# Optimization experiments

Hardware: AMD Instinct MI355X
Metric: run time of the kernel (lower is better)

Reference implementation:

```python
import jax, jax.numpy as jnp
import numpy as np

WS, OWS, HEADS, DH = 8, 12, 4, 16
INNER = HEADS * DH
DIM = 64
RATIO = 0.5
REL = 12  # rel_size = WS + (OWS - WS)


def _conv1x1(x, W, b):
    return jnp.einsum('oc,bchw->bohw', W, x) + b[None, :, None, None]


def _lrelu(x):
    return jnp.where(x >= 0, x, 0.1 * x)


def _rel_to_abs(x):
    # x: [b, l, 2r-1] -> [b, l, r]
    b, l, m = x.shape
    r = (m + 1) // 2
    x = jnp.pad(x, ((0, 0), (0, 0), (0, 1))).reshape(b, l * (m + 1))
    x = jnp.pad(x, ((0, 0), (0, m - l))).reshape(b, l + 1, m)
    return x[:, :l, -r:]


def _relative_logits_1d(q, rel_k):
    # q: [b, h, w, d], rel_k: [2r-1, d] -> [b, h, r, w, r]
    b, h, w, _ = q.shape
    r = (rel_k.shape[0] + 1) // 2
    logits = jnp.einsum('bxyd,rd->bxyr', q, rel_k)
    logits = _rel_to_abs(logits.reshape(b * h, w, 2 * r - 1)).reshape(b, h, w, r)
    return jnp.broadcast_to(logits[:, :, None], (b, h, r, w, r))


def _rel_pos_emb(q, rel_h, rel_w):
    # q: [b, WS*WS, DH] -> [b, WS*WS, REL*REL]
    b = q.shape[0]
    q = q.reshape(b, WS, WS, DH)
    lw = _relative_logits_1d(q, rel_w)                        # [b, x, i, y, j]
    lw = lw.transpose(0, 1, 3, 2, 4).reshape(b, WS * WS, REL * REL)   # (x y),(i j)
    lh = _relative_logits_1d(q.transpose(0, 2, 1, 3), rel_h)  # [b, y, i, x, j]
    lh = lh.transpose(0, 3, 1, 4, 2).reshape(b, WS * WS, REL * REL)   # (x y),(j i)
    return lw + lh


def _windows(t, B, Hw, Ww):
    # 'b c (h p1) (w p2) -> b (h w) (p1 p2 c)'
    return t.reshape(B, INNER, Hw, WS, Ww, WS).transpose(0, 2, 4, 3, 5, 1).reshape(B, Hw * Ww, WS * WS * INNER)


def _forward(x, condition_global, Wq, bq, Wk, bk, Wv, bv, Wout, bout,
             rel_h, rel_w, pin_W, pin_b, ln_w, ln_b, sa_W, sa_b,
             m1_W, m1_b, m2_W, m2_b):
    B, C, H, W = x.shape
    Hw, Ww = H // WS, W // WS
    Nw = Hw * Ww
    keep = int(Nw * RATIO)  # deterministic num_keep_node (expected r=0.5)
    scale = DH ** -0.5

    qs = _conv1x1(x, Wq, bq)
    ks = _conv1x1(x, Wk, bk)
    vs = _conv1x1(x, Wv, bv)

    # condition_wind: stacked ij meshgrid of linspace(-1,1,WS), tiled over windows
    lin = jnp.linspace(-1.0, 1.0, WS)
    gy, gx = jnp.meshgrid(lin, lin, indexing='ij')
    wind = jnp.tile(jnp.stack([gy, gx]).astype(x.dtype)[None], (B, 1, Hw, Ww))
    cond = jnp.concatenate([vs, condition_global, wind], axis=1)  # [B, INNER+4, H, W]

    # PredictorLG
    h1 = _conv1x1(cond, pin_W, pin_b)
    u = h1.mean(1, keepdims=True)
    s = ((h1 - u) ** 2).mean(1, keepdims=True)
    h1 = ln_w[None, :, None, None] * (h1 - u) / jnp.sqrt(s + 1e-6) + ln_b[None, :, None, None]
    h1 = _lrelu(h1)
    sa = jax.lax.conv_general_dilated(h1, sa_W, (1, 1), ((1, 1), (1, 1)),
                                      dimension_numbers=('NCHW', 'OIHW', 'NCHW'))
    sa = jax.nn.sigmoid(sa + sa_b[None, :, None, None])          # [B,1,H,W]

    xm = h1.mean(1)                                               # [B,H,W]
    xm = xm.reshape(B, Hw, WS, Ww, WS).transpose(0, 1, 3, 2, 4).reshape(B, Nw, WS * WS)
    z = _lrelu(xm @ m1_W.T + m1_b)
    pred = jax.nn.softmax(z @ m2_W.T + m2_b, axis=-1)
    score = pred[:, :, 0]
    idx = jnp.argsort(-score, axis=1)
    idx1, idx2 = idx[:, :keep], idx[:, keep:]
    bar = jnp.arange(B)[:, None]

    v_easy = vs * sa

    qw = _windows(qs, B, Hw, Ww)                                  # [B, Nw, 64*INNER]

    pad = (OWS - WS) // 2
    def unfold(t):
        p = jax.lax.conv_general_dilated_patches(t, (OWS, OWS), (WS, WS),
                                                 [(pad, pad), (pad, pad)])
        # [B, INNER*OWS*OWS, Hw, Ww], channel-major (c, kh, kw) like torch unfold
        p = p.reshape(B, INNER, OWS * OWS, Nw)
        return p.transpose(0, 3, 2, 1).reshape(B, Nw, OWS * OWS * INNER)  # (j c)
    kw, vw = unfold(ks), unfold(vs)

    qk, kk, vk = qw[bar, idx1], kw[bar, idx1], vw[bar, idx1]       # gather hard windows

    def heads(t, ntok):
        return t.reshape(B * keep, ntok, HEADS, DH).transpose(0, 2, 1, 3).reshape(B * keep * HEADS, ntok, DH)
    qh = heads(qk, WS * WS) * scale
    kh = heads(kk, OWS * OWS)
    vh = heads(vk, OWS * OWS)

    attn = jnp.einsum('bqc,bkc->bqk', qh, kh) + _rel_pos_emb(qh, rel_h, rel_w)
    attn = jax.nn.softmax(attn, axis=-1)
    vo = jnp.einsum('bqk,bkc->bqc', attn, vh)                      # [B*keep*HEADS, 64, DH]

    # '(b j head) (p1 p2) c -> b j (p1 p2 head c)'
    v1 = vo.reshape(B, keep, HEADS, WS * WS, DH).transpose(0, 1, 3, 2, 4).reshape(B, keep, WS * WS * INNER)
    v2 = _windows(v_easy, B, Hw, Ww)[bar, idx2]

    out = jnp.zeros((B, Nw, WS * WS * INNER), x.dtype)
    out = out.at[bar, idx1].set(v1).at[bar, idx2].set(v2)          # batch_index_fill
    # 'b (h w) (dh dw c) -> b c (h dh) (w dw)'
    out = out.reshape(B, Hw, Ww, WS, WS, INNER).transpose(0, 5, 1, 3, 2, 4).reshape(B, INNER, H, W)
    return _conv1x1(out, Wout, bout)


def setup_inputs() -> dict:
    key = jax.random.key(0)
    k = jax.random.split(key, 16)
    B, H, W = 2, 256, 256
    cdim = INNER + 4
    rel_scale = DH ** -0.5

    def p(kk, shape, s=0.05):
        return jax.random.normal(kk, shape, jnp.float32) * s

    return {
        'x': jax.random.normal(k[0], (B, DIM, H, W), jnp.float32),
        'condition_global': jax.random.normal(k[1], (B, 2, H, W), jnp.float32),
        'Wq': p(k[2], (INNER, DIM)), 'bq': jnp.zeros((INNER,), jnp.float32),
        'Wk': p(k[3], (INNER, DIM)), 'bk': jnp.zeros((INNER,), jnp.float32),
        'Wv': p(k[4], (INNER, DIM)), 'bv': jnp.zeros((INNER,), jnp.float32),
        'Wout': p(k[5], (DIM, INNER)), 'bout': jnp.zeros((DIM,), jnp.float32),
        'rel_h': jax.random.normal(k[6], (2 * REL - 1, DH), jnp.float32) * rel_scale,
        'rel_w': jax.random.normal(k[7], (2 * REL - 1, DH), jnp.float32) * rel_scale,
        'pin_W': p(k[8], (cdim // 4, cdim)), 'pin_b': jnp.zeros((cdim // 4,), jnp.float32),
        'ln_w': jnp.ones((cdim // 4,), jnp.float32), 'ln_b': jnp.zeros((cdim // 4,), jnp.float32),
        'sa_W': p(k[9], (1, cdim // 4, 3, 3)), 'sa_b': jnp.zeros((1,), jnp.float32),
        'm1_W': p(k[10], (WS, WS * WS)), 'm1_b': jnp.zeros((WS,), jnp.float32),
        'm2_W': p(k[11], (2, WS)), 'm2_b': jnp.zeros((2,), jnp.float32),
    }


def reference(x, condition_global, Wq, bq, Wk, bk, Wv, bv, Wout, bout,
              rel_h, rel_w, pin_W, pin_b, ln_w, ln_b, sa_W, sa_b,
              m1_W, m1_b, m2_W, m2_b):
    return _forward(x, condition_global, Wq, bq, Wk, bk, Wv, bv, Wout, bout,
                    rel_h, rel_w, pin_W, pin_b, ln_w, ln_b, sa_W, sa_b,
                    m1_W, m1_b, m2_W, m2_b)
```

## Files before the change

### kernel.cpp

```cpp
#include <hip/hip_runtime.h>
#include <math.h>

#define NPIX   65536
#define NPIXT  131072
#define NW     1024
#define KEEP   512
#define PITCH  68


__global__ __launch_bounds__(256) void k_qkv(
    const float* __restrict__ x,
    const float* __restrict__ Wq, const float* __restrict__ bq,
    const float* __restrict__ Wk, const float* __restrict__ bk,
    const float* __restrict__ Wv, const float* __restrict__ bv,
    float* __restrict__ qs, float* __restrict__ ks, float* __restrict__ vs)
{
    __shared__ float xs[64][64];
    const int tid  = threadIdx.x;
    const int px   = tid & 63;
    const int og   = __builtin_amdgcn_readfirstlane(tid >> 6);
    const int tile = blockIdx.x;
    const int b    = tile >> 10;
    const int p0   = (tile & 1023) << 6;
    const int gp   = (b << 16) + p0 + px;

    #pragma unroll
    for (int it = 0; it < 4; ++it) {
        const int i = it * 256 + tid;
        const int c = i >> 4;
        const int f = i & 15;
        *(float4*)&xs[c][f * 4] =
            *(const float4*)(x + ((size_t)(b * 64 + c)) * NPIX + p0 + f * 4);
    }
    __syncthreads();

    const float* Ws[3]   = {Wq, Wk, Wv};
    const float* bias[3] = {bq, bk, bv};
    float* outs[3] = {qs + (size_t)gp * 64, ks + (size_t)gp * 64, vs + (size_t)gp * 64};

    float acc[3][16];
    #pragma unroll
    for (int m = 0; m < 3; ++m)
        #pragma unroll
        for (int j = 0; j < 16; ++j) acc[m][j] = 0.f;

    #pragma unroll 2
    for (int c = 0; c < 64; ++c) {
        const float xv = xs[c][px];
        #pragma unroll
        for (int m = 0; m < 3; ++m) {
            const float* W = Ws[m];
            #pragma unroll
            for (int j = 0; j < 16; ++j)
                acc[m][j] += W[(og * 16 + j) * 64 + c] * xv;
        }
    }
    #pragma unroll
    for (int m = 0; m < 3; ++m) {
        const float* bb = bias[m];
        #pragma unroll
        for (int j4 = 0; j4 < 4; ++j4) {
            float4 v;
            v.x = acc[m][j4 * 4 + 0] + bb[og * 16 + j4 * 4 + 0];
            v.y = acc[m][j4 * 4 + 1] + bb[og * 16 + j4 * 4 + 1];
            v.z = acc[m][j4 * 4 + 2] + bb[og * 16 + j4 * 4 + 2];
            v.w = acc[m][j4 * 4 + 3] + bb[og * 16 + j4 * 4 + 3];
            *(float4*)(outs[m] + og * 16 + j4 * 4) = v;
        }
    }
}

__global__ __launch_bounds__(256) void k_cond(
    const float* __restrict__ vs, const float* __restrict__ cg,
    const float* __restrict__ pinW, const float* __restrict__ pinb,
    const float* __restrict__ lnw, const float* __restrict__ lnb,
    float* __restrict__ h1, float* __restrict__ xm)
{
    const int gp = blockIdx.x * 256 + threadIdx.x;
    const int b  = gp >> 16;
    const int p  = gp & 65535;
    const int h  = p >> 8;
    const int w  = p & 255;

    float acc[17];
    #pragma unroll
    for (int oc = 0; oc < 17; ++oc) acc[oc] = pinb[oc];

    const float* vp = vs + (size_t)gp * 64;
    #pragma unroll 4
    for (int c4 = 0; c4 < 16; ++c4) {
        const float4 v4 = *(const float4*)(vp + c4 * 4);
        const float vv[4] = {v4.x, v4.y, v4.z, v4.w};
        #pragma unroll
        for (int k = 0; k < 4; ++k) {
            const int c = c4 * 4 + k;
            #pragma unroll
            for (int oc = 0; oc < 17; ++oc)
                acc[oc] += pinW[oc * 68 + c] * vv[k];
        }
    }
    const float c64 = cg[(b * 2 + 0) * NPIX + p];
    const float c65 = cg[(b * 2 + 1) * NPIX + p];
    const float c66 = -1.f + 2.f * (float)(h & 7) / 7.f;
    const float c67 = -1.f + 2.f * (float)(w & 7) / 7.f;
    #pragma unroll
    for (int oc = 0; oc < 17; ++oc)
        acc[oc] += pinW[oc * 68 + 64] * c64 + pinW[oc * 68 + 65] * c65 +
                   pinW[oc * 68 + 66] * c66 + pinW[oc * 68 + 67] * c67;

    float u = 0.f;
    #pragma unroll
    for (int oc = 0; oc < 17; ++oc) u += acc[oc];
    u *= (1.f / 17.f);
    float s = 0.f;
    #pragma unroll
    for (int oc = 0; oc < 17; ++oc) { const float d = acc[oc] - u; s += d * d; }
    s *= (1.f / 17.f);
    const float rstd = rsqrtf(s + 1e-6f);

    float xsum = 0.f;
    #pragma unroll
    for (int oc = 0; oc < 17; ++oc) {
        float hv = lnw[oc] * (acc[oc] - u) * rstd + lnb[oc];
        hv = (hv >= 0.f) ? hv : 0.1f * hv;
        h1[(b * 17 + oc) * NPIX + p] = hv;
        xsum += hv;
    }
    xm[gp] = xsum * (1.f / 17.f);
}

__global__ __launch_bounds__(256) void k_sa(
    const float* __restrict__ h1, const float* __restrict__ saW,
    const float* __restrict__ sab, float* __restrict__ sa)
{
    __shared__ float S[17 * 3 * 256];
    const int tid = threadIdx.x;
    const int b   = blockIdx.x >> 8;
    const int row = blockIdx.x & 255;

    for (int i = tid; i < 3264; i += 256) {
        const int ch  = i / 192;
        const int rem = i - ch * 192;
        const int dr  = rem >> 6;
        const int c4  = rem & 63;
        const int rr  = row + dr - 1;
        float4 v = {0.f, 0.f, 0.f, 0.f};
        if ((unsigned)rr < 256u)
            v = *(const float4*)(h1 + ((size_t)(b * 17 + ch)) * NPIX + rr * 256 + c4 * 4);
        *(float4*)&S[(ch * 3 + dr) * 256 + c4 * 4] = v;
    }
    __syncthreads();

    const int w = tid;
    float acc = sab[0];
    #pragma unroll 1
    for (int ch = 0; ch < 17; ++ch) {
        #pragma unroll
        for (int dr = 0; dr < 3; ++dr) {
            const float* Sp = &S[(ch * 3 + dr) * 256];
            const float m  = Sp[w];
            const float l  = (w > 0)   ? Sp[w - 1] : 0.f;
            const float r_ = (w < 255) ? Sp[w + 1] : 0.f;
            const float* Wp = saW + (ch * 3 + dr) * 3;
            acc += Wp[0] * l + Wp[1] * m + Wp[2] * r_;
        }
    }
    sa[b * NPIX + row * 256 + w] = 1.f / (1.f + __expf(-acc));
}

__global__ __launch_bounds__(1024) void k_score_select(
    const float* __restrict__ xm,
    const float* __restrict__ m1W, const float* __restrict__ m1b,
    const float* __restrict__ m2W, const float* __restrict__ m2b,
    int* __restrict__ flag, int* __restrict__ kept)
{
    __shared__ float sc[NW];
    const int b = blockIdx.x;
    const int t = threadIdx.x;
    const int i = t >> 5;
    const int j = t & 31;

    float z[8];
    #pragma unroll
    for (int jj = 0; jj < 8; ++jj) z[jj] = m1b[jj];

    for (int a = 0; a < 8; ++a) {
        #pragma unroll
        for (int cc = 0; cc < 8; ++cc) {
            const float xv = xm[b * NPIX + (i * 8 + a) * 256 + (j * 8 + cc)];
            const int tt = a * 8 + cc;
            #pragma unroll
            for (int jj = 0; jj < 8; ++jj)
                z[jj] += m1W[jj * 64 + tt] * xv;
        }
    }
    #pragma unroll
    for (int jj = 0; jj < 8; ++jj) z[jj] = (z[jj] >= 0.f) ? z[jj] : 0.1f * z[jj];

    float l0 = m2b[0], l1 = m2b[1];
    #pragma unroll
    for (int jj = 0; jj < 8; ++jj) { l0 += m2W[jj] * z[jj]; l1 += m2W[8 + jj] * z[jj]; }
    const float mx = fmaxf(l0, l1);
    const float e0 = expf(l0 - mx), e1 = expf(l1 - mx);
    sc[t] = e0 / (e0 + e1);
    __syncthreads();

    const float s = sc[t];
    int cnt = 0;
    for (int jq = 0; jq < NW; ++jq) {
        const float sj = sc[jq];
        cnt += (sj > s) || (sj == s && jq < t);
    }
    flag[b * NW + t] = (cnt < KEEP) ? 1 : 0;
    if (cnt < KEEP) kept[b * KEEP + cnt] = t;
}

__global__ __launch_bounds__(256) void k_attn(
    const float* __restrict__ qs, const float* __restrict__ ks,
    const float* __restrict__ vs, const int* __restrict__ kept,
    const float* __restrict__ relh, const float* __restrict__ relw,
    float* __restrict__ amix)
{
    __shared__ float SK[72 * PITCH];
    __shared__ float SV[72 * PITCH];

    const int b    = blockIdx.y;
    const int win  = kept[b * KEEP + blockIdx.x];
    const int wy = win >> 5, wx = win & 31;
    const int tid  = threadIdx.x;
    const int head = tid >> 6;
    const int lane = tid & 63;
    const int choff = head * 16;
    const size_t bbase = (size_t)b * NPIX;
    const int px0 = (wy * 8) * 256 + wx * 8;

    #pragma unroll
    for (int it = 0; it < 4; ++it) {
        const int i  = it * 256 + tid;
        const int px = i >> 4;
        const int c4 = i & 15;
        const float4 v = *(const float4*)(
            qs + (bbase + px0 + (px >> 3) * 256 + (px & 7)) * 64 + c4 * 4);
        *(float4*)&SK[px * PITCH + c4 * 4] = v;
    }
    __syncthreads();

    const int qrow = lane >> 3, qcol = lane & 7;
    float q[16];
    #pragma unroll
    for (int j4 = 0; j4 < 4; ++j4) {
        const float4 v = *(const float4*)&SK[(qrow * 8 + qcol) * PITCH + choff + j4 * 4];
        q[j4 * 4 + 0] = v.x * 0.25f; q[j4 * 4 + 1] = v.y * 0.25f;
        q[j4 * 4 + 2] = v.z * 0.25f; q[j4 * 4 + 3] = v.w * 0.25f;
    }

    float cw[12];
    #pragma unroll
    for (int k = 0; k < 12; ++k) {
        const float* rw = relw + (k - qcol + 11) * 16;
        float sw = 0.f;
        #pragma unroll
        for (int j4 = 0; j4 < 4; ++j4) {
            const float4 w4 = *(const float4*)(rw + j4 * 4);
            sw += q[j4*4+0]*w4.x + q[j4*4+1]*w4.y + q[j4*4+2]*w4.z + q[j4*4+3]*w4.w;
        }
        cw[k] = sw;
    }

    const int wy8 = wy * 8 - 2, wx8 = wx * 8 - 2;

    float sum = 0.f;
    float vo[16];
    #pragma unroll
    for (int d = 0; d < 16; ++d) vo[d] = 0.f;

    #pragma unroll 1
    for (int c = 0; c < 2; ++c) {
        __syncthreads();
        for (int i = tid; i < 1152; i += 256) {
            const int pxl = i >> 4;
            const int c4  = i & 15;
            const int rl  = pxl / 12;
            const int col = pxl - rl * 12;
            const int ry  = wy8 + 6 * c + rl;
            const int cx  = wx8 + col;
            float4 kv = {0.f,0.f,0.f,0.f}, vv = {0.f,0.f,0.f,0.f};
            if ((unsigned)ry < 256u && (unsigned)cx < 256u) {
                const size_t g = (bbase + ry * 256 + cx) * 64 + c4 * 4;
                kv = *(const float4*)(ks + g);
                vv = *(const float4*)(vs + g);
            }
            *(float4*)&SK[pxl * PITCH + c4 * 4] = kv;
            *(float4*)&SV[pxl * PITCH + c4 * 4] = vv;
        }
        __syncthreads();

        #pragma unroll 1
        for (int rl = 0; rl < 6; ++rl) {
            const float* rh = relh + (c * 6 + rl - qrow + 11) * 16;
            float srow = 0.f;
            #pragma unroll
            for (int j4 = 0; j4 < 4; ++j4) {
                const float4 h4 = *(const float4*)(rh + j4 * 4);
                srow += q[j4*4+0]*h4.x + q[j4*4+1]*h4.y + q[j4*4+2]*h4.z + q[j4*4+3]*h4.w;
            }

            const float* kbase = &SK[(rl * 12) * PITCH + choff];
            const float* vbase = &SV[(rl * 12) * PITCH + choff];
            #pragma unroll
            for (int col = 0; col < 12; ++col) {
                const float* kb = kbase + col * PITCH;
                const float4 k0 = *(const float4*)(kb + 0);
                const float4 k1 = *(const float4*)(kb + 4);
                const float4 k2 = *(const float4*)(kb + 8);
                const float4 k3 = *(const float4*)(kb + 12);
                float s = srow + cw[col];
                s += k0.x*q[0];  s += k0.y*q[1];  s += k0.z*q[2];  s += k0.w*q[3];
                s += k1.x*q[4];  s += k1.y*q[5];  s += k1.z*q[6];  s += k1.w*q[7];
                s += k2.x*q[8];  s += k2.y*q[9];  s += k2.z*q[10]; s += k2.w*q[11];
                s += k3.x*q[12]; s += k3.y*q[13]; s += k3.z*q[14]; s += k3.w*q[15];
                const float e = __expf(s);
                sum += e;
                const float* vb = vbase + col * PITCH;
                const float4 v0 = *(const float4*)(vb + 0);
                const float4 v1 = *(const float4*)(vb + 4);
                const float4 v2 = *(const float4*)(vb + 8);
                const float4 v3 = *(const float4*)(vb + 12);
                vo[0]  += e*v0.x; vo[1]  += e*v0.y; vo[2]  += e*v0.z; vo[3]  += e*v0.w;
                vo[4]  += e*v1.x; vo[5]  += e*v1.y; vo[6]  += e*v1.z; vo[7]  += e*v1.w;
                vo[8]  += e*v2.x; vo[9]  += e*v2.y; vo[10] += e*v2.z; vo[11] += e*v2.w;
                vo[12] += e*v3.x; vo[13] += e*v3.y; vo[14] += e*v3.z; vo[15] += e*v3.w;
            }
        }
    }

    const float inv = 1.f / sum;
    __syncthreads();
    #pragma unroll
    for (int j4 = 0; j4 < 4; ++j4) {
        float4 v;
        v.x = vo[j4*4+0] * inv; v.y = vo[j4*4+1] * inv;
        v.z = vo[j4*4+2] * inv; v.w = vo[j4*4+3] * inv;
        *(float4*)&SK[(qrow * 8 + qcol) * PITCH + choff + j4 * 4] = v;
    }
    __syncthreads();
    #pragma unroll
    for (int it = 0; it < 4; ++it) {
        const int i  = it * 256 + tid;
        const int px = i >> 4;
        const int c4 = i & 15;
        const float4 v = *(const float4*)&SK[px * PITCH + c4 * 4];
        *(float4*)(amix + (bbase + px0 + (px >> 3) * 256 + (px & 7)) * 64 + c4 * 4) = v;
    }
}

__global__ __launch_bounds__(256) void k_out_f(
    const float* __restrict__ amix, const float* __restrict__ vs,
    const float* __restrict__ sa, const int* __restrict__ flag,
    const float* __restrict__ W, const float* __restrict__ bias,
    float* __restrict__ out)
{
    __shared__ float xs[64][65];
    __shared__ float smult[64];
    __shared__ int   sflag[64];
    const int tid  = threadIdx.x;
    const int px   = tid & 63;
    const int og   = __builtin_amdgcn_readfirstlane(tid >> 6);
    const int tile = blockIdx.x;
    const int b    = tile >> 10;
    const int p0   = (tile & 1023) << 6;
    const int p    = p0 + px;
    const int gp   = (b << 16) + p;

    {
        const int h   = p >> 8, w = p & 255;
        const int win = (h >> 3) * 32 + (w >> 3);
        const int fl  = flag[b * NW + win];
        sflag[px] = fl;
        smult[px] = fl ? 1.f : sa[gp];
    }
    __syncthreads();

    #pragma unroll
    for (int it = 0; it < 4; ++it) {
        const int i   = it * 256 + tid;
        const int pxl = i >> 4;
        const int c4  = i & 15;
        const int gpl = (b << 16) + p0 + pxl;
        const float* src = (sflag[pxl] ? amix : vs) + (size_t)gpl * 64;
        const float m = smult[pxl];
        const float4 v = *(const float4*)(src + c4 * 4);
        xs[c4 * 4 + 0][pxl] = v.x * m;
        xs[c4 * 4 + 1][pxl] = v.y * m;
        xs[c4 * 4 + 2][pxl] = v.z * m;
        xs[c4 * 4 + 3][pxl] = v.w * m;
    }
    __syncthreads();

    float acc[16];
    #pragma unroll
    for (int j = 0; j < 16; ++j) acc[j] = 0.f;
    #pragma unroll 2
    for (int c = 0; c < 64; ++c) {
        const float xv = xs[c][px];
        #pragma unroll
        for (int j = 0; j < 16; ++j)
            acc[j] += W[(og * 16 + j) * 64 + c] * xv;
    }

    const int base = (b << 6) * NPIX + p;
    #pragma unroll
    for (int j = 0; j < 16; ++j)
        out[base + (og * 16 + j) * NPIX] = acc[j] + bias[og * 16 + j];
}

extern "C" void kernel_launch(void* const* d_in, const int* in_sizes, int n_in,
                              void* d_out, int out_size, void* d_ws, size_t ws_size,
                              hipStream_t stream)
{
    const float* x    = (const float*)d_in[0];
    const float* cg   = (const float*)d_in[1];
    const float* Wq   = (const float*)d_in[2];
    const float* bq   = (const float*)d_in[3];
    const float* Wk   = (const float*)d_in[4];
    const float* bk   = (const float*)d_in[5];
    const float* Wv   = (const float*)d_in[6];
    const float* bv   = (const float*)d_in[7];
    const float* Wout = (const float*)d_in[8];
    const float* bout = (const float*)d_in[9];
    const float* relh = (const float*)d_in[10];
    const float* relw = (const float*)d_in[11];
    const float* pinW = (const float*)d_in[12];
    const float* pinb = (const float*)d_in[13];
    const float* lnw  = (const float*)d_in[14];
    const float* lnb  = (const float*)d_in[15];
    const float* saW  = (const float*)d_in[16];
    const float* sab  = (const float*)d_in[17];
    const float* m1W  = (const float*)d_in[18];
    const float* m1b  = (const float*)d_in[19];
    const float* m2W  = (const float*)d_in[20];
    const float* m2b  = (const float*)d_in[21];
    float* out = (float*)d_out;

    float* ws    = (float*)d_ws;
    float* qs    = ws;
    float* ks    = qs + 8388608;
    float* vs    = ks + 8388608;
    float* h1    = vs + 8388608;
    float* xm    = h1 + 17 * NPIXT;
    float* sa    = xm + NPIXT;
    int*   flag  = (int*)(sa + NPIXT);
    int*   kept  = flag + 2048;

    k_qkv         <<<2048, 256, 0, stream>>>(x, Wq, bq, Wk, bk, Wv, bv, qs, ks, vs);
    k_cond        <<<NPIXT / 256, 256, 0, stream>>>(vs, cg, pinW, pinb, lnw, lnb, h1, xm);
    k_sa          <<<512, 256, 0, stream>>>(h1, saW, sab, sa);
    k_score_select<<<2, 1024, 0, stream>>>(xm, m1W, m1b, m2W, m2b, flag, kept);
    k_attn        <<<dim3(KEEP, 2), 256, 0, stream>>>(qs, ks, vs, kept, relh, relw, qs);
    k_out_f       <<<2048, 256, 0, stream>>>(qs, vs, sa, flag, Wout, bout, out);
}
```

Measured before the change: 377.4 us.

## Stage transposed weights in LDS, shrink attention LDS, vectorize top-k ranking

The QKV and output projections now transpose the weight matrix into shared memory and read it as float4 rows. Before, each thread issued scalar global (or scalar-cache) weight loads. The QKV kernel also streams x straight from global with register prefetch instead of staging a tile. The attention kernel loads q directly from global and splits the K/V halo into four smaller chunks, halving shared memory so more blocks can be resident. The top-k ranking loop reads scores as float4, and one unroll factor is raised. Costs are extra barriers per chunk, and the QKV path now reads x from global three times and reloads weights per matrix.

```diff
diff --git a/kernel.cpp b/kernel.cpp
--- a/kernel.cpp
+++ b/kernel.cpp
@@ -15,7 +15,7 @@
     const float* __restrict__ Wv, const float* __restrict__ bv,
     float* __restrict__ qs, float* __restrict__ ks, float* __restrict__ vs)
 {
-    __shared__ float xs[64][64];
+    __shared__ float Wt[64][68];
     const int tid  = threadIdx.x;
     const int px   = tid & 63;
     const int og   = __builtin_amdgcn_readfirstlane(tid >> 6);
@@ -24,48 +24,74 @@
     const int p0   = (tile & 1023) << 6;
     const int gp   = (b << 16) + p0 + px;
 
-    #pragma unroll
-    for (int it = 0; it < 4; ++it) {
-        const int i = it * 256 + tid;
-        const int c = i >> 4;
-        const int f = i & 15;
-        *(float4*)&xs[c][f * 4] =
-            *(const float4*)(x + ((size_t)(b * 64 + c)) * NPIX + p0 + f * 4);
-    }
-    __syncthreads();
-
     const float* Ws[3]   = {Wq, Wk, Wv};
     const float* bias[3] = {bq, bk, bv};
     float* outs[3] = {qs + (size_t)gp * 64, ks + (size_t)gp * 64, vs + (size_t)gp * 64};
-
-    float acc[3][16];
-    #pragma unroll
-    for (int m = 0; m < 3; ++m)
-        #pragma unroll
-        for (int j = 0; j < 16; ++j) acc[m][j] = 0.f;
-
-    #pragma unroll 2
-    for (int c = 0; c < 64; ++c) {
-        const float xv = xs[c][px];
-        #pragma unroll
-        for (int m = 0; m < 3; ++m) {
-            const float* W = Ws[m];
+    const float* xg = x + ((size_t)b * 64) * NPIX + p0 + px;
+    const int wo = og * 16;
+
+    #pragma unroll
+    for (int m = 0; m < 3; ++m) {
+        __syncthreads();
+        const float* Wm = Ws[m];
+        #pragma unroll
+        for (int it = 0; it < 4; ++it) {
+            const int i  = it * 256 + tid;
+            const int o  = i >> 4;
+            const int c4 = i & 15;
+            const float4 w = *(const float4*)(Wm + o * 64 + c4 * 4);
+            Wt[c4 * 4 + 0][o] = w.x;
+            Wt[c4 * 4 + 1][o] = w.y;
+            Wt[c4 * 4 + 2][o] = w.z;
+            Wt[c4 * 4 + 3][o] = w.w;
+        }
+        __syncthreads();
+
+        float acc[16];
+        #pragma unroll
+        for (int j = 0; j < 16; ++j) acc[j] = 0.f;
+
+        float xr[8];
+        #pragma unroll
+        for (int k = 0; k < 8; ++k) xr[k] = xg[(size_t)k * NPIX];
+
+        #pragma unroll 2
+        for (int cb = 0; cb < 64; cb += 8) {
+            float xn[8];
+            if (cb + 8 < 64) {
+                #pragma unroll
+                for (int k = 0; k < 8; ++k) xn[k] = xg[(size_t)(cb + 8 + k) * NPIX];
+            }
             #pragma unroll
-            for (int j = 0; j < 16; ++j)
-                acc[m][j] += W[(og * 16 + j) * 64 + c] * xv;
-        }
-    }
-    #pragma unroll
-    for (int m = 0; m < 3; ++m) {
+            for (int k = 0; k < 8; ++k) {
+                const int c = cb + k;
+                const float xv = xr[k];
+                const float4 w0 = *(const float4*)&Wt[c][wo + 0];
+                const float4 w1 = *(const float4*)&Wt[c][wo + 4];
+                const float4 w2 = *(const float4*)&Wt[c][wo + 8];
+                const float4 w3 = *(const float4*)&Wt[c][wo + 12];
+                acc[0]  += w0.x * xv; acc[1]  += w0.y * xv;
+                acc[2]  += w0.z * xv; acc[3]  += w0.w * xv;
+                acc[4]  += w1.x * xv; acc[5]  += w1.y * xv;
+                acc[6]  += w1.z * xv; acc[7]  += w1.w * xv;
+                acc[8]  += w2.x * xv; acc[9]  += w2.y * xv;
+                acc[10] += w2.z * xv; acc[11] += w2.w * xv;
+                acc[12] += w3.x * xv; acc[13] += w3.y * xv;
+                acc[14] += w3.z * xv; acc[15] += w3.w * xv;
+            }
+            #pragma unroll
+            for (int k = 0; k < 8; ++k) xr[k] = xn[k];
+        }
+
         const float* bb = bias[m];
         #pragma unroll
         for (int j4 = 0; j4 < 4; ++j4) {
             float4 v;
-            v.x = acc[m][j4 * 4 + 0] + bb[og * 16 + j4 * 4 + 0];
-            v.y = acc[m][j4 * 4 + 1] + bb[og * 16 + j4 * 4 + 1];
-            v.z = acc[m][j4 * 4 + 2] + bb[og * 16 + j4 * 4 + 2];
-            v.w = acc[m][j4 * 4 + 3] + bb[og * 16 + j4 * 4 + 3];
-            *(float4*)(outs[m] + og * 16 + j4 * 4) = v;
+            v.x = acc[j4 * 4 + 0] + bb[wo + j4 * 4 + 0];
+            v.y = acc[j4 * 4 + 1] + bb[wo + j4 * 4 + 1];
+            v.z = acc[j4 * 4 + 2] + bb[wo + j4 * 4 + 2];
+            v.w = acc[j4 * 4 + 3] + bb[wo + j4 * 4 + 3];
+            *(float4*)(outs[m] + wo + j4 * 4) = v;
         }
     }
 }
@@ -87,7 +113,7 @@
     for (int oc = 0; oc < 17; ++oc) acc[oc] = pinb[oc];
 
     const float* vp = vs + (size_t)gp * 64;
-    #pragma unroll 4
+    #pragma unroll 8
     for (int c4 = 0; c4 < 16; ++c4) {
         const float4 v4 = *(const float4*)(vp + c4 * 4);
         const float vv[4] = {v4.x, v4.y, v4.z, v4.w};
@@ -207,9 +233,12 @@
 
     const float s = sc[t];
     int cnt = 0;
-    for (int jq = 0; jq < NW; ++jq) {
-        const float sj = sc[jq];
-        cnt += (sj > s) || (sj == s && jq < t);
+    for (int jq = 0; jq < NW; jq += 4) {
+        const float4 s4 = *(const float4*)&sc[jq];
+        cnt += (s4.x > s) || (s4.x == s && (jq + 0) < t);
+        cnt += (s4.y > s) || (s4.y == s && (jq + 1) < t);
+        cnt += (s4.z > s) || (s4.z == s && (jq + 2) < t);
+        cnt += (s4.w > s) || (s4.w == s && (jq + 3) < t);
     }
     flag[b * NW + t] = (cnt < KEEP) ? 1 : 0;
     if (cnt < KEEP) kept[b * KEEP + cnt] = t;
@@ -221,8 +250,9 @@
     const float* __restrict__ relh, const float* __restrict__ relw,
     float* __restrict__ amix)
 {
-    __shared__ float SK[72 * PITCH];
-    __shared__ float SV[72 * PITCH];
+    __shared__ float S[2 * 36 * PITCH];
+    float* SK = S;
+    float* SV = S + 36 * PITCH;
 
     const int b    = blockIdx.y;
     const int win  = kept[b * KEEP + blockIdx.x];
@@ -233,25 +263,17 @@
     const int choff = head * 16;
     const size_t bbase = (size_t)b * NPIX;
     const int px0 = (wy * 8) * 256 + wx * 8;
-
-    #pragma unroll
-    for (int it = 0; it < 4; ++it) {
-        const int i  = it * 256 + tid;
-        const int px = i >> 4;
-        const int c4 = i & 15;
-        const float4 v = *(const float4*)(
-            qs + (bbase + px0 + (px >> 3) * 256 + (px & 7)) * 64 + c4 * 4);
-        *(float4*)&SK[px * PITCH + c4 * 4] = v;
-    }
-    __syncthreads();
-
     const int qrow = lane >> 3, qcol = lane & 7;
+
     float q[16];
-    #pragma unroll
-    for (int j4 = 0; j4 < 4; ++j4) {
-        const float4 v = *(const float4*)&SK[(qrow * 8 + qcol) * PITCH + choff + j4 * 4];
-        q[j4 * 4 + 0] = v.x * 0.25f; q[j4 * 4 + 1] = v.y * 0.25f;
-        q[j4 * 4 + 2] = v.z * 0.25f; q[j4 * 4 + 3] = v.w * 0.25f;
+    {
+        const float* qp = qs + (bbase + px0 + qrow * 256 + qcol) * 64 + choff;
+        #pragma unroll
+        for (int j4 = 0; j4 < 4; ++j4) {
+            const float4 v = *(const float4*)(qp + j4 * 4);
+            q[j4 * 4 + 0] = v.x * 0.25f; q[j4 * 4 + 1] = v.y * 0.25f;
+            q[j4 * 4 + 2] = v.z * 0.25f; q[j4 * 4 + 3] = v.w * 0.25f;
+        }
     }
 
     float cw[12];
@@ -275,14 +297,14 @@
     for (int d = 0; d < 16; ++d) vo[d] = 0.f;
 
     #pragma unroll 1
-    for (int c = 0; c < 2; ++c) {
+    for (int cc = 0; cc < 4; ++cc) {
         __syncthreads();
-        for (int i = tid; i < 1152; i += 256) {
+        for (int i = tid; i < 576; i += 256) {
             const int pxl = i >> 4;
             const int c4  = i & 15;
             const int rl  = pxl / 12;
             const int col = pxl - rl * 12;
-            const int ry  = wy8 + 6 * c + rl;
+            const int ry  = wy8 + 3 * cc + rl;
             const int cx  = wx8 + col;
             float4 kv = {0.f,0.f,0.f,0.f}, vv = {0.f,0.f,0.f,0.f};
             if ((unsigned)ry < 256u && (unsigned)cx < 256u) {
@@ -296,8 +318,8 @@
         __syncthreads();
 
         #pragma unroll 1
-        for (int rl = 0; rl < 6; ++rl) {
-            const float* rh = relh + (c * 6 + rl - qrow + 11) * 16;
+        for (int rl = 0; rl < 3; ++rl) {
+            const float* rh = relh + (3 * cc + rl - qrow + 11) * 16;
             float srow = 0.f;
             #pragma unroll
             for (int j4 = 0; j4 < 4; ++j4) {
@@ -341,7 +363,7 @@
         float4 v;
         v.x = vo[j4*4+0] * inv; v.y = vo[j4*4+1] * inv;
         v.z = vo[j4*4+2] * inv; v.w = vo[j4*4+3] * inv;
-        *(float4*)&SK[(qrow * 8 + qcol) * PITCH + choff + j4 * 4] = v;
+        *(float4*)&S[(qrow * 8 + qcol) * PITCH + choff + j4 * 4] = v;
     }
     __syncthreads();
     #pragma unroll
@@ -349,7 +371,7 @@
         const int i  = it * 256 + tid;
         const int px = i >> 4;
         const int c4 = i & 15;
-        const float4 v = *(const float4*)&SK[px * PITCH + c4 * 4];
+        const float4 v = *(const float4*)&S[px * PITCH + c4 * 4];
         *(float4*)(amix + (bbase + px0 + (px >> 3) * 256 + (px & 7)) * 64 + c4 * 4) = v;
     }
 }
@@ -361,6 +383,7 @@
     float* __restrict__ out)
 {
     __shared__ float xs[64][65];
+    __shared__ float Wt[64][68];
     __shared__ float smult[64];
     __shared__ int   sflag[64];
     const int tid  = threadIdx.x;
@@ -371,10 +394,23 @@
     const int p0   = (tile & 1023) << 6;
     const int p    = p0 + px;
     const int gp   = (b << 16) + p;
+    const int wo   = og * 16;
+
+    #pragma unroll
+    for (int it = 0; it < 4; ++it) {
+        const int i  = it * 256 + tid;
+        const int o  = i >> 4;
+        const int c4 = i & 15;
+        const float4 w = *(const float4*)(W + o * 64 + c4 * 4);
+        Wt[c4 * 4 + 0][o] = w.x;
+        Wt[c4 * 4 + 1][o] = w.y;
+        Wt[c4 * 4 + 2][o] = w.z;
+        Wt[c4 * 4 + 3][o] = w.w;
+    }
 
     {
-        const int h   = p >> 8, w = p & 255;
-        const int win = (h >> 3) * 32 + (w >> 3);
+        const int h   = p >> 8, w_ = p & 255;
+        const int win = (h >> 3) * 32 + (w_ >> 3);
         const int fl  = flag[b * NW + win];
         sflag[px] = fl;
         smult[px] = fl ? 1.f : sa[gp];
@@ -400,18 +436,27 @@
     float acc[16];
     #pragma unroll
     for (int j = 0; j < 16; ++j) acc[j] = 0.f;
-    #pragma unroll 2
+    #pragma unroll 4
     for (int c = 0; c < 64; ++c) {
         const float xv = xs[c][px];
-        #pragma unroll
-        for (int j = 0; j < 16; ++j)
-            acc[j] += W[(og * 16 + j) * 64 + c] * xv;
+        const float4 w0 = *(const float4*)&Wt[c][wo + 0];
+        const float4 w1 = *(const float4*)&Wt[c][wo + 4];
+        const float4 w2 = *(const float4*)&Wt[c][wo + 8];
+        const float4 w3 = *(const float4*)&Wt[c][wo + 12];
+        acc[0]  += w0.x * xv; acc[1]  += w0.y * xv;
+        acc[2]  += w0.z * xv; acc[3]  += w0.w * xv;
+        acc[4]  += w1.x * xv; acc[5]  += w1.y * xv;
+        acc[6]  += w1.z * xv; acc[7]  += w1.w * xv;
+        acc[8]  += w2.x * xv; acc[9]  += w2.y * xv;
+        acc[10] += w2.z * xv; acc[11] += w2.w * xv;
+        acc[12] += w3.x * xv; acc[13] += w3.y * xv;
+        acc[14] += w3.z * xv; acc[15] += w3.w * xv;
     }
 
     const int base = (b << 6) * NPIX + p;
     #pragma unroll
     for (int j = 0; j < 16; ++j)
-        out[base + (og * 16 + j) * NPIX] = acc[j] + bias[og * 16 + j];
+        out[base + (wo + j) * NPIX] = acc[j] + bias[wo + j];
 }
 
 extern "C" void kernel_launch(void* const* d_in, const int* in_sizes, int n_in,
```

Result: faster. 366.4 us (-2.9%).

## Rework QKV, attention and output kernels with lane-broadcast weights and two pixels per thread

Applied to the files above, without the earlier changes.

The QKV and output projections now hold weights in registers and broadcast them across the wavefront with readlane. Each thread computes two pixels, and QKV reads x directly from global memory instead of staging it in LDS. Attention moves to one 64-thread block per head, drops its LDS staging, and loads K/V per lane and broadcasts them via readlane. xm is written in window-major order so score selection can use float4 loads, and the rank loop is vectorised. These changes aim to cut LDS traffic and syncs, at the risk of many scalar readlane operations and less coalesced K/V loads.

```diff
diff --git a/kernel.cpp b/kernel.cpp
--- a/kernel.cpp
+++ b/kernel.cpp
@@ -5,8 +5,11 @@
 #define NPIXT  131072
 #define NW     1024
 #define KEEP   512
-#define PITCH  68
-
+
+
+__device__ __forceinline__ float bcast(float v, int l) {
+    return __int_as_float(__builtin_amdgcn_readlane(__float_as_int(v), l));
+}
 
 __global__ __launch_bounds__(256) void k_qkv(
     const float* __restrict__ x,
@@ -15,57 +18,54 @@
     const float* __restrict__ Wv, const float* __restrict__ bv,
     float* __restrict__ qs, float* __restrict__ ks, float* __restrict__ vs)
 {
-    __shared__ float xs[64][64];
     const int tid  = threadIdx.x;
-    const int px   = tid & 63;
+    const int lane = tid & 63;
     const int og   = __builtin_amdgcn_readfirstlane(tid >> 6);
     const int tile = blockIdx.x;
-    const int b    = tile >> 10;
-    const int p0   = (tile & 1023) << 6;
-    const int gp   = (b << 16) + p0 + px;
-
-    #pragma unroll
-    for (int it = 0; it < 4; ++it) {
-        const int i = it * 256 + tid;
-        const int c = i >> 4;
-        const int f = i & 15;
-        *(float4*)&xs[c][f * 4] =
-            *(const float4*)(x + ((size_t)(b * 64 + c)) * NPIX + p0 + f * 4);
-    }
-    __syncthreads();
+    const int b    = tile >> 9;
+    const int p0   = (tile & 511) << 7;
+    const int p    = p0 + 2 * lane;
+    const int gp   = (b << 16) + p;
+    const int wo   = og * 16;
 
     const float* Ws[3]   = {Wq, Wk, Wv};
     const float* bias[3] = {bq, bk, bv};
     float* outs[3] = {qs + (size_t)gp * 64, ks + (size_t)gp * 64, vs + (size_t)gp * 64};
-
-    float acc[3][16];
-    #pragma unroll
-    for (int m = 0; m < 3; ++m)
-        #pragma unroll
-        for (int j = 0; j < 16; ++j) acc[m][j] = 0.f;
-
-    #pragma unroll 2
-    for (int c = 0; c < 64; ++c) {
-        const float xv = xs[c][px];
-        #pragma unroll
-        for (int m = 0; m < 3; ++m) {
-            const float* W = Ws[m];
+    const float* xg = x + ((size_t)b * 64) * NPIX + p;
+
+    #pragma unroll
+    for (int m = 0; m < 3; ++m) {
+        const float* Wm = Ws[m];
+        float w[16];
+        #pragma unroll
+        for (int j = 0; j < 16; ++j) w[j] = Wm[(wo + j) * 64 + lane];
+
+        float acc0[16], acc1[16];
+        #pragma unroll
+        for (int j = 0; j < 16; ++j) { acc0[j] = 0.f; acc1[j] = 0.f; }
+
+        #pragma unroll 8
+        for (int c = 0; c < 64; ++c) {
+            const float2 xv = *(const float2*)(xg + (size_t)c * NPIX);
             #pragma unroll
-            for (int j = 0; j < 16; ++j)
-                acc[m][j] += W[(og * 16 + j) * 64 + c] * xv;
-        }
-    }
-    #pragma unroll
-    for (int m = 0; m < 3; ++m) {
+            for (int j = 0; j < 16; ++j) {
+                const float wv = bcast(w[j], c);
+                acc0[j] += wv * xv.x;
+                acc1[j] += wv * xv.y;
+            }
+        }
+
         const float* bb = bias[m];
+        float* o0 = outs[m];
         #pragma unroll
         for (int j4 = 0; j4 < 4; ++j4) {
-            float4 v;
-            v.x = acc[m][j4 * 4 + 0] + bb[og * 16 + j4 * 4 + 0];
-            v.y = acc[m][j4 * 4 + 1] + bb[og * 16 + j4 * 4 + 1];
-            v.z = acc[m][j4 * 4 + 2] + bb[og * 16 + j4 * 4 + 2];
-            v.w = acc[m][j4 * 4 + 3] + bb[og * 16 + j4 * 4 + 3];
-            *(float4*)(outs[m] + og * 16 + j4 * 4) = v;
+            float4 v0, v1;
+            v0.x = acc0[j4*4+0] + bb[wo + j4*4+0]; v1.x = acc1[j4*4+0] + bb[wo + j4*4+0];
+            v0.y = acc0[j4*4+1] + bb[wo + j4*4+1]; v1.y = acc1[j4*4+1] + bb[wo + j4*4+1];
+            v0.z = acc0[j4*4+2] + bb[wo + j4*4+2]; v1.z = acc1[j4*4+2] + bb[wo + j4*4+2];
+            v0.w = acc0[j4*4+3] + bb[wo + j4*4+3]; v1.w = acc1[j4*4+3] + bb[wo + j4*4+3];
+            *(float4*)(o0 + wo + j4*4)      = v0;
+            *(float4*)(o0 + 64 + wo + j4*4) = v1;
         }
     }
 }
@@ -87,7 +87,7 @@
     for (int oc = 0; oc < 17; ++oc) acc[oc] = pinb[oc];
 
     const float* vp = vs + (size_t)gp * 64;
-    #pragma unroll 4
+    #pragma unroll 8
     for (int c4 = 0; c4 < 16; ++c4) {
         const float4 v4 = *(const float4*)(vp + c4 * 4);
         const float vv[4] = {v4.x, v4.y, v4.z, v4.w};
@@ -126,7 +126,9 @@
         h1[(b * 17 + oc) * NPIX + p] = hv;
         xsum += hv;
     }
-    xm[gp] = xsum * (1.f / 17.f);
+    const int win = (h >> 3) * 32 + (w >> 3);
+    const int idx = ((h & 7) << 3) | (w & 7);
+    xm[(b << 16) + win * 64 + idx] = xsum * (1.f / 17.f);
 }
 
 __global__ __launch_bounds__(256) void k_sa(
@@ -177,21 +179,22 @@
     __shared__ float sc[NW];
     const int b = blockIdx.x;
     const int t = threadIdx.x;
-    const int i = t >> 5;
-    const int j = t & 31;
 
     float z[8];
     #pragma unroll
     for (int jj = 0; jj < 8; ++jj) z[jj] = m1b[jj];
 
-    for (int a = 0; a < 8; ++a) {
-        #pragma unroll
-        for (int cc = 0; cc < 8; ++cc) {
-            const float xv = xm[b * NPIX + (i * 8 + a) * 256 + (j * 8 + cc)];
-            const int tt = a * 8 + cc;
+    const float* xw = xm + (b << 16) + t * 64;
+    #pragma unroll 4
+    for (int t4 = 0; t4 < 16; ++t4) {
+        const float4 v4 = *(const float4*)(xw + t4 * 4);
+        const float vv[4] = {v4.x, v4.y, v4.z, v4.w};
+        #pragma unroll
+        for (int k = 0; k < 4; ++k) {
+            const int tt = t4 * 4 + k;
             #pragma unroll
             for (int jj = 0; jj < 8; ++jj)
-                z[jj] += m1W[jj * 64 + tt] * xv;
+                z[jj] += m1W[jj * 64 + tt] * vv[k];
         }
     }
     #pragma unroll
@@ -207,51 +210,43 @@
 
     const float s = sc[t];
     int cnt = 0;
-    for (int jq = 0; jq < NW; ++jq) {
-        const float sj = sc[jq];
-        cnt += (sj > s) || (sj == s && jq < t);
+    for (int jq = 0; jq < NW; jq += 4) {
+        const float4 s4 = *(const float4*)&sc[jq];
+        cnt += (s4.x > s) || (s4.x == s && (jq + 0) < t);
+        cnt += (s4.y > s) || (s4.y == s && (jq + 1) < t);
+        cnt += (s4.z > s) || (s4.z == s && (jq + 2) < t);
+        cnt += (s4.w > s) || (s4.w == s && (jq + 3) < t);
     }
     flag[b * NW + t] = (cnt < KEEP) ? 1 : 0;
     if (cnt < KEEP) kept[b * KEEP + cnt] = t;
 }
 
-__global__ __launch_bounds__(256) void k_attn(
+__global__ __launch_bounds__(64) void k_attn(
     const float* __restrict__ qs, const float* __restrict__ ks,
     const float* __restrict__ vs, const int* __restrict__ kept,
     const float* __restrict__ relh, const float* __restrict__ relw,
     float* __restrict__ amix)
 {
-    __shared__ float SK[72 * PITCH];
-    __shared__ float SV[72 * PITCH];
-
-    const int b    = blockIdx.y;
+    const int b    = blockIdx.z;
+    const int head = blockIdx.y;
     const int win  = kept[b * KEEP + blockIdx.x];
     const int wy = win >> 5, wx = win & 31;
-    const int tid  = threadIdx.x;
-    const int head = tid >> 6;
-    const int lane = tid & 63;
+    const int lane = threadIdx.x;
     const int choff = head * 16;
     const size_t bbase = (size_t)b * NPIX;
     const int px0 = (wy * 8) * 256 + wx * 8;
-
-    #pragma unroll
-    for (int it = 0; it < 4; ++it) {
-        const int i  = it * 256 + tid;
-        const int px = i >> 4;
-        const int c4 = i & 15;
-        const float4 v = *(const float4*)(
-            qs + (bbase + px0 + (px >> 3) * 256 + (px & 7)) * 64 + c4 * 4);
-        *(float4*)&SK[px * PITCH + c4 * 4] = v;
-    }
-    __syncthreads();
-
     const int qrow = lane >> 3, qcol = lane & 7;
+    const int sub = lane >> 4, d_ = lane & 15;
+
     float q[16];
-    #pragma unroll
-    for (int j4 = 0; j4 < 4; ++j4) {
-        const float4 v = *(const float4*)&SK[(qrow * 8 + qcol) * PITCH + choff + j4 * 4];
-        q[j4 * 4 + 0] = v.x * 0.25f; q[j4 * 4 + 1] = v.y * 0.25f;
-        q[j4 * 4 + 2] = v.z * 0.25f; q[j4 * 4 + 3] = v.w * 0.25f;
+    {
+        const float* qp = qs + (bbase + px0 + qrow * 256 + qcol) * 64 + choff;
+        #pragma unroll
+        for (int j4 = 0; j4 < 4; ++j4) {
+            const float4 v = *(const float4*)(qp + j4 * 4);
+            q[j4 * 4 + 0] = v.x * 0.25f; q[j4 * 4 + 1] = v.y * 0.25f;
+            q[j4 * 4 + 2] = v.z * 0.25f; q[j4 * 4 + 3] = v.w * 0.25f;
+        }
     }
 
     float cw[12];
@@ -268,6 +263,7 @@
     }
 
     const int wy8 = wy * 8 - 2, wx8 = wx * 8 - 2;
+    const int laneoff = choff + d_;
 
     float sum = 0.f;
     float vo[16];
@@ -275,82 +271,50 @@
     for (int d = 0; d < 16; ++d) vo[d] = 0.f;
 
     #pragma unroll 1
-    for (int c = 0; c < 2; ++c) {
-        __syncthreads();
-        for (int i = tid; i < 1152; i += 256) {
-            const int pxl = i >> 4;
-            const int c4  = i & 15;
-            const int rl  = pxl / 12;
-            const int col = pxl - rl * 12;
-            const int ry  = wy8 + 6 * c + rl;
-            const int cx  = wx8 + col;
-            float4 kv = {0.f,0.f,0.f,0.f}, vv = {0.f,0.f,0.f,0.f};
-            if ((unsigned)ry < 256u && (unsigned)cx < 256u) {
-                const size_t g = (bbase + ry * 256 + cx) * 64 + c4 * 4;
-                kv = *(const float4*)(ks + g);
-                vv = *(const float4*)(vs + g);
+    for (int r = 0; r < 12; ++r) {
+        const int ry = wy8 + r;
+        const bool rowok = (unsigned)ry < 256u;
+
+        const float* rh = relh + (r - qrow + 11) * 16;
+        float srow = 0.f;
+        #pragma unroll
+        for (int j4 = 0; j4 < 4; ++j4) {
+            const float4 h4 = *(const float4*)(rh + j4 * 4);
+            srow += q[j4*4+0]*h4.x + q[j4*4+1]*h4.y + q[j4*4+2]*h4.z + q[j4*4+3]*h4.w;
+        }
+
+        #pragma unroll
+        for (int gi = 0; gi < 3; ++gi) {
+            const int cx = wx8 + 4 * gi + sub;
+            float kg = 0.f, vg = 0.f;
+            if (rowok && (unsigned)cx < 256u) {
+                const size_t a = (bbase + (size_t)(ry * 256 + cx)) * 64 + laneoff;
+                kg = ks[a];
+                vg = vs[a];
             }
-            *(float4*)&SK[pxl * PITCH + c4 * 4] = kv;
-            *(float4*)&SV[pxl * PITCH + c4 * 4] = vv;
-        }
-        __syncthreads();
-
-        #pragma unroll 1
-        for (int rl = 0; rl < 6; ++rl) {
-            const float* rh = relh + (c * 6 + rl - qrow + 11) * 16;
-            float srow = 0.f;
             #pragma unroll
-            for (int j4 = 0; j4 < 4; ++j4) {
-                const float4 h4 = *(const float4*)(rh + j4 * 4);
-                srow += q[j4*4+0]*h4.x + q[j4*4+1]*h4.y + q[j4*4+2]*h4.z + q[j4*4+3]*h4.w;
-            }
-
-            const float* kbase = &SK[(rl * 12) * PITCH + choff];
-            const float* vbase = &SV[(rl * 12) * PITCH + choff];
-            #pragma unroll
-            for (int col = 0; col < 12; ++col) {
-                const float* kb = kbase + col * PITCH;
-                const float4 k0 = *(const float4*)(kb + 0);
-                const float4 k1 = *(const float4*)(kb + 4);
-                const float4 k2 = *(const float4*)(kb + 8);
-                const float4 k3 = *(const float4*)(kb + 12);
-                float s = srow + cw[col];
-                s += k0.x*q[0];  s += k0.y*q[1];  s += k0.z*q[2];  s += k0.w*q[3];
-                s += k1.x*q[4];  s += k1.y*q[5];  s += k1.z*q[6];  s += k1.w*q[7];
-                s += k2.x*q[8];  s += k2.y*q[9];  s += k2.z*q[10]; s += k2.w*q[11];
-                s += k3.x*q[12]; s += k3.y*q[13]; s += k3.z*q[14]; s += k3.w*q[15];
+            for (int kk = 0; kk < 4; ++kk) {
+                float s = srow + cw[4 * gi + kk];
+                #pragma unroll
+                for (int d = 0; d < 16; ++d)
+                    s += bcast(kg, kk * 16 + d) * q[d];
                 const float e = __expf(s);
                 sum += e;
-                const float* vb = vbase + col * PITCH;
-                const float4 v0 = *(const float4*)(vb + 0);
-                const float4 v1 = *(const float4*)(vb + 4);
-                const float4 v2 = *(const float4*)(vb + 8);
-                const float4 v3 = *(const float4*)(vb + 12);
-                vo[0]  += e*v0.x; vo[1]  += e*v0.y; vo[2]  += e*v0.z; vo[3]  += e*v0.w;
-                vo[4]  += e*v1.x; vo[5]  += e*v1.y; vo[6]  += e*v1.z; vo[7]  += e*v1.w;
-                vo[8]  += e*v2.x; vo[9]  += e*v2.y; vo[10] += e*v2.z; vo[11] += e*v2.w;
-                vo[12] += e*v3.x; vo[13] += e*v3.y; vo[14] += e*v3.z; vo[15] += e*v3.w;
+                #pragma unroll
+                for (int d = 0; d < 16; ++d)
+                    vo[d] += e * bcast(vg, kk * 16 + d);
             }
         }
     }
 
     const float inv = 1.f / sum;
-    __syncthreads();
+    float* op = amix + (bbase + px0 + qrow * 256 + qcol) * 64 + choff;
     #pragma unroll
     for (int j4 = 0; j4 < 4; ++j4) {
         float4 v;
         v.x = vo[j4*4+0] * inv; v.y = vo[j4*4+1] * inv;
         v.z = vo[j4*4+2] * inv; v.w = vo[j4*4+3] * inv;
-        *(float4*)&SK[(qrow * 8 + qcol) * PITCH + choff + j4 * 4] = v;
-    }
-    __syncthreads();
-    #pragma unroll
-    for (int it = 0; it < 4; ++it) {
-        const int i  = it * 256 + tid;
-        const int px = i >> 4;
-        const int c4 = i & 15;
-        const float4 v = *(const float4*)&SK[px * PITCH + c4 * 4];
-        *(float4*)(amix + (bbase + px0 + (px >> 3) * 256 + (px & 7)) * 64 + c4 * 4) = v;
+        *(float4*)(op + j4 * 4) = v;
     }
 }
 
@@ -360,29 +324,29 @@
     const float* __restrict__ W, const float* __restrict__ bias,
     float* __restrict__ out)
 {
-    __shared__ float xs[64][65];
-    __shared__ float smult[64];
-    __shared__ int   sflag[64];
+    __shared__ float xs[64][130];
+    __shared__ float smult[128];
+    __shared__ int   sflag[128];
     const int tid  = threadIdx.x;
-    const int px   = tid & 63;
+    const int lane = tid & 63;
     const int og   = __builtin_amdgcn_readfirstlane(tid >> 6);
     const int tile = blockIdx.x;
-    const int b    = tile >> 10;
-    const int p0   = (tile & 1023) << 6;
-    const int p    = p0 + px;
-    const int gp   = (b << 16) + p;
-
-    {
-        const int h   = p >> 8, w = p & 255;
-        const int win = (h >> 3) * 32 + (w >> 3);
+    const int b    = tile >> 9;
+    const int p0   = (tile & 511) << 7;
+    const int wo   = og * 16;
+
+    if (tid < 128) {
+        const int p   = p0 + tid;
+        const int h   = p >> 8, w_ = p & 255;
+        const int win = (h >> 3) * 32 + (w_ >> 3);
         const int fl  = flag[b * NW + win];
-        sflag[px] = fl;
-        smult[px] = fl ? 1.f : sa[gp];
+        sflag[tid] = fl;
+        smult[tid] = fl ? 1.f : sa[(b << 16) + p];
     }
     __syncthreads();
 
     #pragma unroll
-    for (int it = 0; it < 4; ++it) {
+    for (int it = 0; it < 8; ++it) {
         const int i   = it * 256 + tid;
         const int pxl = i >> 4;
         const int c4  = i & 15;
@@ -397,21 +361,33 @@
     }
     __syncthreads();
 
-    float acc[16];
-    #pragma unroll
-    for (int j = 0; j < 16; ++j) acc[j] = 0.f;
-    #pragma unroll 2
+    float w[16];
+    #pragma unroll
+    for (int j = 0; j < 16; ++j) w[j] = W[(wo + j) * 64 + lane];
+
+    float acc0[16], acc1[16];
+    #pragma unroll
+    for (int j = 0; j < 16; ++j) { acc0[j] = 0.f; acc1[j] = 0.f; }
+
+    #pragma unroll 8
     for (int c = 0; c < 64; ++c) {
-        const float xv = xs[c][px];
-        #pragma unroll
-        for (int j = 0; j < 16; ++j)
-            acc[j] += W[(og * 16 + j) * 64 + c] * xv;
-    }
-
+        const float2 xv = *(const float2*)&xs[c][2 * lane];
+        #pragma unroll
+        for (int j = 0; j < 16; ++j) {
+            const float wv = bcast(w[j], c);
+            acc0[j] += wv * xv.x;
+            acc1[j] += wv * xv.y;
+        }
+    }
+
+    const int p    = p0 + 2 * lane;
     const int base = (b << 6) * NPIX + p;
     #pragma unroll
-    for (int j = 0; j < 16; ++j)
-        out[base + (og * 16 + j) * NPIX] = acc[j] + bias[og * 16 + j];
+    for (int j = 0; j < 16; ++j) {
+        const float bj = bias[wo + j];
+        out[base +     (wo + j) * NPIX] = acc0[j] + bj;
+        out[base + 1 + (wo + j) * NPIX] = acc1[j] + bj;
+    }
 }
 
 extern "C" void kernel_launch(void* const* d_in, const int* in_sizes, int n_in,
@@ -452,10 +428,10 @@
     int*   flag  = (int*)(sa + NPIXT);
     int*   kept  = flag + 2048;
 
-    k_qkv         <<<2048, 256, 0, stream>>>(x, Wq, bq, Wk, bk, Wv, bv, qs, ks, vs);
+    k_qkv         <<<1024, 256, 0, stream>>>(x, Wq, bq, Wk, bk, Wv, bv, qs, ks, vs);
     k_cond        <<<NPIXT / 256, 256, 0, stream>>>(vs, cg, pinW, pinb, lnw, lnb, h1, xm);
     k_sa          <<<512, 256, 0, stream>>>(h1, saW, sab, sa);
     k_score_select<<<2, 1024, 0, stream>>>(xm, m1W, m1b, m2W, m2b, flag, kept);
-    k_attn        <<<dim3(KEEP, 2), 256, 0, stream>>>(qs, ks, vs, kept, relh, relw, qs);
-    k_out_f       <<<2048, 256, 0, stream>>>(qs, vs, sa, flag, Wout, bout, out);
-}
+    k_attn        <<<dim3(KEEP, 4, 2), 64, 0, stream>>>(qs, ks, vs, kept, relh, relw, qs);
+    k_out_f       <<<1024, 256, 0, stream>>>(qs, vs, sa, flag, Wout, bout, out);
+}
```

Result: slower. 441.3 us (+17.0%).
